# Kernel tuning notes

Measured on AMD Instinct MI355X. Metric: run time of the kernel, lower is better.

Reference implementation:

```python
import jax, jax.numpy as jnp
import numpy as np

B, K, D = 16384, 5, 512
HG = 16  # WeightGate hidden dim
BN_EPS = 1e-5
NORM_EPS = 1e-12  # F.normalize eps


def setup_inputs() -> dict:
    key = jax.random.key(0)
    ks = jax.random.split(key, 10)
    n = jax.random.normal
    s = 0.05
    return {
        "image_embedding": n(ks[0], (B, D), dtype=jnp.float32),
        "text_embeddings": n(ks[1], (B, K, D), dtype=jnp.float32),
        # WeightGate: Linear(1,16) -> ReLU -> Linear(16,1) -> Sigmoid
        "wg_w1": n(ks[2], (1, HG)) * s, "wg_b1": jnp.zeros((HG,)),
        "wg_w2": n(ks[3], (HG, 1)) * s, "wg_b2": jnp.zeros((1,)),
        # MergeGate: Conv2d(1,1,(K,1)) + BN(512) -> Linear(512,512) -> GELU
        "conv_w": n(ks[4], (K,)) * s, "conv_b": jnp.zeros(()),
        "mg_bn_g": jnp.ones((D,)), "mg_bn_b": jnp.zeros((D,)),
        "mg_w": n(ks[5], (D, D)) * s, "mg_b": jnp.zeros((D,)),
        # ProjectionHead (shared for image & text): BN->Linear->GELU->BN->Linear
        "ph_bn1_g": jnp.ones((D,)), "ph_bn1_b": jnp.zeros((D,)),
        "ph_w1": n(ks[6], (D, D)) * s, "ph_b1": jnp.zeros((D,)),
        "ph_bn2_g": jnp.ones((D,)), "ph_bn2_b": jnp.zeros((D,)),
        "ph_w2": n(ks[7], (D, D)) * s, "ph_b2": jnp.zeros((D,)),
    }


def _batchnorm(x, g, b):
    # training-mode BatchNorm1d: batch mean, biased variance
    m = jnp.mean(x, axis=0)
    v = jnp.var(x, axis=0)
    return (x - m) * jax.lax.rsqrt(v + BN_EPS) * g + b


def _l2norm_rows(x):
    return x / jnp.sqrt(jnp.sum(x * x, axis=1, keepdims=True))


def _forward(image_embedding, text_embeddings,
             wg_w1, wg_b1, wg_w2, wg_b2,
             conv_w, conv_b, mg_bn_g, mg_bn_b, mg_w, mg_b,
             ph_bn1_g, ph_bn1_b, ph_w1, ph_b1, ph_bn2_g, ph_bn2_b, ph_w2, ph_b2):
    # cosine similarity: [B, K]
    img_n = image_embedding / jnp.maximum(
        jnp.linalg.norm(image_embedding, axis=-1, keepdims=True), NORM_EPS)
    txt_n = text_embeddings / jnp.maximum(
        jnp.linalg.norm(text_embeddings, axis=-1, keepdims=True), NORM_EPS)
    sim = jnp.einsum("bd,bkd->bk", img_n, txt_n)

    # WeightGate: per-scalar tiny MLP
    h = jax.nn.relu(sim[..., None] * wg_w1[0] + wg_b1)        # [B, K, HG]
    weights = jax.nn.sigmoid(h @ wg_w2 + wg_b2)[..., 0]       # [B, K]

    weighted = text_embeddings * weights[..., None]           # [B, K, D]

    # sort by weight (descending) and gather
    idx = jnp.argsort(-weights, axis=1)                       # [B, K]
    sorted_txt = jnp.take_along_axis(weighted, idx[..., None], axis=1)

    # MergeGate: (K,1) conv collapses K -> scalar weighted sum over K
    x = jnp.einsum("bkd,k->bd", sorted_txt, conv_w) + conv_b  # [B, D]
    # dropout is identity in eval mode
    fused = jax.nn.gelu(_batchnorm(x, mg_bn_g, mg_bn_b) @ mg_w + mg_b)

    def proj(z):
        z = jax.nn.gelu(_batchnorm(z, ph_bn1_g, ph_bn1_b) @ ph_w1 + ph_b1)
        z = _batchnorm(z, ph_bn2_g, ph_bn2_b) @ ph_w2 + ph_b2
        return _l2norm_rows(z)

    return proj(image_embedding), proj(fused)


def reference(image_embedding, text_embeddings,
              wg_w1, wg_b1, wg_w2, wg_b2,
              conv_w, conv_b, mg_bn_g, mg_bn_b, mg_w, mg_b,
              ph_bn1_g, ph_bn1_b, ph_w1, ph_b1, ph_bn2_g, ph_bn2_b, ph_w2, ph_b2):
    return _forward(image_embedding, text_embeddings,
                    wg_w1, wg_b1, wg_w2, wg_b2,
                    conv_w, conv_b, mg_bn_g, mg_bn_b, mg_w, mg_b,
                    ph_bn1_g, ph_bn1_b, ph_w1, ph_b1,
                    ph_bn2_g, ph_bn2_b, ph_w2, ph_b2)
```

## Files before the change

kernel.cpp:

```cpp
#include <hip/hip_runtime.h>
#include <cmath>

#define NROWS 16384
#define DDIM  512

typedef __attribute__((ext_vector_type(8))) short          bf16x8;
typedef __attribute__((ext_vector_type(4))) float          f32x4;
typedef __attribute__((ext_vector_type(8))) unsigned short u16x8;
typedef __attribute__((ext_vector_type(4))) unsigned short u16x4;

__device__ __forceinline__ unsigned short f2bf(float f) {
  unsigned u = __float_as_uint(f);
  u += 0x7fffu + ((u >> 16) & 1u);
  return (unsigned short)(u >> 16);
}

__device__ __forceinline__ float gelu_tanh(float x) {
  float x3 = x * x * x;
  float t = tanhf(0.79788456080286535588f * (x + 0.044715f * x3));
  return 0.5f * x * (1.0f + t);
}

__device__ __forceinline__ void ld8(const float* p, float* v) {
  float4 a = *(const float4*)p;
  float4 b = *(const float4*)(p + 256);
  v[0] = a.x; v[1] = a.y; v[2] = a.z; v[3] = a.w;
  v[4] = b.x; v[5] = b.y; v[6] = b.z; v[7] = b.w;
}

__device__ __forceinline__ void st8(float* p, const float* v) {
  *(float4*)p = make_float4(v[0], v[1], v[2], v[3]);
  *(float4*)(p + 256) = make_float4(v[4], v[5], v[6], v[7]);
}

__device__ __forceinline__ float wave_sum(float v) {
#pragma unroll
  for (int m = 1; m < 64; m <<= 1) v += __shfl_xor(v, m, 64);
  return v;
}

__device__ __forceinline__ void gload_lds16(const void* g, void* l) {
  __builtin_amdgcn_global_load_lds(
      (const __attribute__((address_space(1))) unsigned int*)g,
      (__attribute__((address_space(3))) unsigned int*)l, 16, 0, 0);
}

__global__ __launch_bounds__(256) void prep_kernel(
    const float* __restrict__ img, const float* __restrict__ txt,
    const float* __restrict__ wg_w1, const float* __restrict__ wg_b1,
    const float* __restrict__ wg_w2, const float* __restrict__ wg_b2,
    const float* __restrict__ conv_w, const float* __restrict__ conv_b,
    unsigned short* __restrict__ xbf, unsigned short* __restrict__ imgbf,
    float* __restrict__ accPart) {
  __shared__ float csX[512], cqX[512], csI[512], cqI[512];
  const int tid = threadIdx.x;
  for (int i = tid; i < 512; i += 256) {
    csX[i] = 0.f; cqX[i] = 0.f; csI[i] = 0.f; cqI[i] = 0.f;
  }
  __syncthreads();

  const int lane = tid & 63;
  const int gwave = blockIdx.x * 4 + (tid >> 6);

  const float cb = conv_b[0];
  const float b2f = wg_b2[0];
  float w1f[16], b1f[16], w2f[16];
#pragma unroll
  for (int i = 0; i < 16; i++) {
    w1f[i] = wg_w1[i]; b1f[i] = wg_b1[i]; w2f[i] = wg_w2[i];
  }
  float cw[5];
#pragma unroll
  for (int k = 0; k < 5; k++) cw[k] = conv_w[k];

  float sX[8] = {0, 0, 0, 0, 0, 0, 0, 0}, qX[8] = {0, 0, 0, 0, 0, 0, 0, 0};
  float sI[8] = {0, 0, 0, 0, 0, 0, 0, 0}, qI[8] = {0, 0, 0, 0, 0, 0, 0, 0};

  for (int it = 0; it < 8; it++) {
    const int r = gwave * 8 + it;
    const float* ip = img + (size_t)r * DDIM + lane * 4;
    float iv[8];
    ld8(ip, iv);

    {
      u16x4 lo, hi;
#pragma unroll
      for (int j = 0; j < 4; j++) { lo[j] = f2bf(iv[j]); hi[j] = f2bf(iv[4 + j]); }
      *(u16x4*)(imgbf + (size_t)r * DDIM + lane * 4) = lo;
      *(u16x4*)(imgbf + (size_t)r * DDIM + 256 + lane * 4) = hi;
    }
#pragma unroll
    for (int j = 0; j < 8; j++) { sI[j] += iv[j]; qI[j] += iv[j] * iv[j]; }

    float tv[5][8];
#pragma unroll
    for (int k = 0; k < 5; k++)
      ld8(txt + ((size_t)r * 5 + k) * DDIM + lane * 4, tv[k]);

    double ss = 0.0;
    double s2[5], dp[5];
#pragma unroll
    for (int k = 0; k < 5; k++) { s2[k] = 0.0; dp[k] = 0.0; }
#pragma unroll
    for (int j = 0; j < 8; j++) {
      ss += (double)iv[j] * (double)iv[j];
#pragma unroll
      for (int k = 0; k < 5; k++) {
        s2[k] += (double)tv[k][j] * (double)tv[k][j];
        dp[k] += (double)iv[j] * (double)tv[k][j];
      }
    }

#pragma unroll
    for (int m = 1; m < 64; m <<= 1) {
      ss += __shfl_xor(ss, m, 64);
#pragma unroll
      for (int k = 0; k < 5; k++) {
        s2[k] += __shfl_xor(s2[k], m, 64);
        dp[k] += __shfl_xor(dp[k], m, 64);
      }
    }
    const double dimg = fmax(sqrt(ss), 1e-12);

    double simv[5];
#pragma unroll
    for (int k = 0; k < 5; k++) {
      const double dt = fmax(sqrt(s2[k]), 1e-12);
      simv[k] = dp[k] / (dimg * dt);
    }

    double o[5];
#pragma unroll
    for (int k = 0; k < 5; k++) o[k] = (double)b2f;
#pragma unroll
    for (int i = 0; i < 16; i++) {
      const double w1d = (double)w1f[i];
      const double b1d = (double)b1f[i];
      const double w2d = (double)w2f[i];
#pragma unroll
      for (int k = 0; k < 5; k++) {
        double h = simv[k] * w1d + b1d;
        h = fmax(h, 0.0);
        o[k] += h * w2d;
      }
    }
    float wv[5];
#pragma unroll
    for (int k = 0; k < 5; k++) {
      float o32 = (float)o[k];
      float e32 = (float)exp(-(double)o32);
      float a32 = 1.0f + e32;
      wv[k] = 1.0f / a32;
    }

    float c[5];
#pragma unroll
    for (int k = 0; k < 5; k++) {
      int rk = 0;
#pragma unroll
      for (int j = 0; j < 5; j++)
        rk += (int)((wv[j] > wv[k]) || ((wv[j] == wv[k]) && (j < k)));
      c[k] = cw[rk] * wv[k];
    }

    float xv[8];
#pragma unroll
    for (int j = 0; j < 8; j++) {
      float v = cb;
#pragma unroll
      for (int k = 0; k < 5; k++) v = fmaf(c[k], tv[k][j], v);
      xv[j] = v;
    }
    {
      u16x4 lo, hi;
#pragma unroll
      for (int j = 0; j < 4; j++) { lo[j] = f2bf(xv[j]); hi[j] = f2bf(xv[4 + j]); }
      *(u16x4*)(xbf + (size_t)r * DDIM + lane * 4) = lo;
      *(u16x4*)(xbf + (size_t)r * DDIM + 256 + lane * 4) = hi;
    }

#pragma unroll
    for (int j = 0; j < 8; j++) { sX[j] += xv[j]; qX[j] += xv[j] * xv[j]; }
  }

  const int c0 = lane * 4, c1 = 256 + lane * 4;
#pragma unroll
  for (int j = 0; j < 4; j++) {
    atomicAdd(&csX[c0 + j], sX[j]);     atomicAdd(&cqX[c0 + j], qX[j]);
    atomicAdd(&csX[c1 + j], sX[4 + j]); atomicAdd(&cqX[c1 + j], qX[4 + j]);
    atomicAdd(&csI[c0 + j], sI[j]);     atomicAdd(&cqI[c0 + j], qI[j]);
    atomicAdd(&csI[c1 + j], sI[4 + j]); atomicAdd(&cqI[c1 + j], qI[4 + j]);
  }
  __syncthreads();
  float* base = accPart + (size_t)(blockIdx.x & 31) * 2048;
  for (int i = tid; i < 512; i += 256) {
    atomicAdd(&base[i], csX[i]);
    atomicAdd(&base[512 + i], cqX[i]);
    atomicAdd(&base[1024 + i], csI[i]);
    atomicAdd(&base[1536 + i], cqI[i]);
  }
}

__global__ __launch_bounds__(256) void wconv_kernel(
    const float* __restrict__ W,
    const float* __restrict__ s, const float* __restrict__ q,
    const float* __restrict__ g, const float* __restrict__ b,
    float invM, int ncopies, int stride,
    unsigned short* __restrict__ Wt, float* __restrict__ addv) {
  __shared__ float T[32][33];
  __shared__ float P[32];
  __shared__ float SC[32], SH[32];
  const int t = threadIdx.x;
  const int k0 = blockIdx.x * 32, n0 = blockIdx.y * 32;
  {
    int r = t >> 3, c = (t & 7) * 4;
    float4 v = *(const float4*)&W[(size_t)(k0 + r) * 512 + n0 + c];
    T[r][c] = v.x; T[r][c + 1] = v.y; T[r][c + 2] = v.z; T[r][c + 3] = v.w;
  }
  if (t < 32) {
    P[t] = 0.f;
    const int j = k0 + t;
    float ss = 0.f, qq = 0.f;
    for (int c = 0; c < ncopies; c++) {
      ss += s[(size_t)c * stride + j];
      qq += q[(size_t)c * stride + j];
    }
    float m = ss * invM;
    float v = qq * invM - m * m;
    float r = 1.0f / sqrtf(v + 1e-5f);
    float sc = g[j] * r;
    SC[t] = sc;
    SH[t] = fmaf(-m, sc, b[j]);
  }
  __syncthreads();
  {
    int n = t >> 3, k = (t & 7) * 4;
    u16x4 o;
#pragma unroll
    for (int i = 0; i < 4; i++) o[i] = f2bf(T[k + i][n] * SC[k + i]);
    *(u16x4*)&Wt[(size_t)(n0 + n) * 512 + k0 + k] = o;
  }
  {
    int n = t & 31, rb = (t >> 5) * 4;
    float p = 0.f;
#pragma unroll
    for (int i = 0; i < 4; i++) p += SH[rb + i] * T[rb + i][n];
    atomicAdd(&P[n], p);
  }
  __syncthreads();
  if (t < 32) atomicAdd(&addv[n0 + t], P[t]);
}

__global__ __launch_bounds__(256) void gemm_bf16(
    const unsigned short* __restrict__ A, const unsigned short* __restrict__ Wt,
    const float* __restrict__ bias, const float* __restrict__ addv,
    float* __restrict__ Cf, unsigned short* __restrict__ Cb, int do_gelu,
    float* __restrict__ accS, float* __restrict__ accQ,
    const unsigned short* __restrict__ A2, const unsigned short* __restrict__ W2,
    const float* __restrict__ bias2, const float* __restrict__ addv2,
    float* __restrict__ Cf2, int mblocks) {
  __shared__ __align__(16) short As[128 * 32];
  __shared__ __align__(16) short Bs[128 * 32];
  __shared__ float colS[128], colQ[128];
  const int tid = threadIdx.x;
  const int ln = tid & 63;
  const int lq = ln >> 4, lr = ln & 15;
  const int wv = tid >> 6;
  const int wm = wv >> 1, wn = wv & 1;

  int bx = blockIdx.x;
  if (A2 && bx >= mblocks) {
    bx -= mblocks;
    A = A2; Wt = W2; bias = bias2; addv = addv2; Cf = Cf2; Cb = nullptr;
  }
  const int bm = bx * 128, bn = blockIdx.y * 128;

  f32x4 acc[4][4];
#pragma unroll
  for (int i = 0; i < 4; i++)
#pragma unroll
    for (int j = 0; j < 4; j++) acc[i][j] = (f32x4){0.f, 0.f, 0.f, 0.f};

  const int idx0 = tid, idx1 = 256 + tid;
  const int r0 = idx0 >> 2, k0g = (idx0 & 3) ^ ((r0 >> 1) & 3);
  const int r1 = idx1 >> 2, k1g = (idx1 & 3) ^ ((r1 >> 1) & 3);
  const unsigned short* ga0 = A + (size_t)(bm + r0) * 512 + k0g * 8;
  const unsigned short* ga1 = A + (size_t)(bm + r1) * 512 + k1g * 8;
  const unsigned short* gb0 = Wt + (size_t)(bn + r0) * 512 + k0g * 8;
  const unsigned short* gb1 = Wt + (size_t)(bn + r1) * 512 + k1g * 8;

  const int wb = (tid >> 6) << 10;
  char* lA0 = (char*)As + wb;
  char* lA1 = (char*)As + 4096 + wb;
  char* lB0 = (char*)Bs + wb;
  char* lB1 = (char*)Bs + 4096 + wb;

  gload_lds16(ga0, lA0); gload_lds16(ga1, lA1);
  gload_lds16(gb0, lB0); gload_lds16(gb1, lB1);

  for (int kk = 0; kk < 512; kk += 32) {
    __syncthreads();
    bf16x8 af[4], bfr[4];
#pragma unroll
    for (int i = 0; i < 4; i++) {
      int r = wm * 64 + i * 16 + lr;
      af[i] = *(const bf16x8*)((const char*)As + r * 64 + ((lq ^ ((r >> 1) & 3)) << 4));
    }
#pragma unroll
    for (int j = 0; j < 4; j++) {
      int n = wn * 64 + j * 16 + lr;
      bfr[j] = *(const bf16x8*)((const char*)Bs + n * 64 + ((lq ^ ((n >> 1) & 3)) << 4));
    }
#pragma unroll
    for (int i = 0; i < 4; i++)
#pragma unroll
      for (int j = 0; j < 4; j++)
        acc[i][j] = __builtin_amdgcn_mfma_f32_16x16x32_bf16(af[i], bfr[j], acc[i][j], 0, 0, 0);
    __syncthreads();
    if (kk + 32 < 512) {
      gload_lds16(ga0 + kk + 32, lA0); gload_lds16(ga1 + kk + 32, lA1);
      gload_lds16(gb0 + kk + 32, lB0); gload_lds16(gb1 + kk + 32, lB1);
    }
  }

  const bool do_stats = (accS != nullptr);
  if (do_stats) {
    if (tid < 128) { colS[tid] = 0.f; colQ[tid] = 0.f; }
    __syncthreads();
  }
  float badd[4];
  int cols[4];
#pragma unroll
  for (int j = 0; j < 4; j++) {
    int c = bn + wn * 64 + j * 16 + lr;
    cols[j] = c;
    badd[j] = bias[c] + addv[c];
  }
#pragma unroll
  for (int j = 0; j < 4; j++) {
    float s = 0.f, q = 0.f;
#pragma unroll
    for (int i = 0; i < 4; i++) {
      int rbase = bm + wm * 64 + i * 16 + lq * 4;
#pragma unroll
      for (int rg = 0; rg < 4; rg++) {
        float v = acc[i][j][rg] + badd[j];
        if (do_gelu) v = gelu_tanh(v);
        size_t off = (size_t)(rbase + rg) * 512 + cols[j];
        if (Cb) Cb[off] = f2bf(v);
        else Cf[off] = v;
        s += v; q += v * v;
      }
    }
    if (do_stats) {
      atomicAdd(&colS[wn * 64 + j * 16 + lr], s);
      atomicAdd(&colQ[wn * 64 + j * 16 + lr], q);
    }
  }
  if (do_stats) {
    __syncthreads();
    if (tid < 128) {
      atomicAdd(&accS[bn + tid], colS[tid]);
      atomicAdd(&accQ[bn + tid], colQ[tid]);
    }
  }
}

__global__ __launch_bounds__(256) void l2norm_kernel(float* __restrict__ out) {
  const int wave = blockIdx.x * 4 + (threadIdx.x >> 6);
  const int lane = threadIdx.x & 63;
  float* p = out + (size_t)wave * DDIM + lane * 4;
  float v[8];
  ld8(p, v);
  float ss = 0.f;
#pragma unroll
  for (int j = 0; j < 8; j++) ss += v[j] * v[j];
  ss = wave_sum(ss);
  const float inv = 1.0f / sqrtf(ss);
#pragma unroll
  for (int j = 0; j < 8; j++) v[j] *= inv;
  st8(p, v);
}

extern "C" void kernel_launch(void* const* d_in, const int* in_sizes, int n_in,
                              void* d_out, int out_size, void* d_ws, size_t ws_size,
                              hipStream_t stream) {
  const float* img     = (const float*)d_in[0];
  const float* txt     = (const float*)d_in[1];
  const float* wg_w1   = (const float*)d_in[2];
  const float* wg_b1   = (const float*)d_in[3];
  const float* wg_w2   = (const float*)d_in[4];
  const float* wg_b2   = (const float*)d_in[5];
  const float* conv_w  = (const float*)d_in[6];
  const float* conv_b  = (const float*)d_in[7];
  const float* mg_bn_g = (const float*)d_in[8];
  const float* mg_bn_b = (const float*)d_in[9];
  const float* mg_w    = (const float*)d_in[10];
  const float* mg_b    = (const float*)d_in[11];
  const float* ph_bn1_g= (const float*)d_in[12];
  const float* ph_bn1_b= (const float*)d_in[13];
  const float* ph_w1   = (const float*)d_in[14];
  const float* ph_b1   = (const float*)d_in[15];
  const float* ph_bn2_g= (const float*)d_in[16];
  const float* ph_bn2_b= (const float*)d_in[17];
  const float* ph_w2   = (const float*)d_in[18];
  const float* ph_b2   = (const float*)d_in[19];
  float* out = (float*)d_out;

  const size_t BD = (size_t)NROWS * DDIM;
  const size_t WSZ = 512 * 512;

  unsigned short* xbf   = (unsigned short*)d_ws;
  unsigned short* imgbf = xbf + BD;
  unsigned short* fusbf = imgbf + BD;
  unsigned short* Wt0   = fusbf + BD;
  unsigned short* Wt1   = Wt0 + WSZ;
  unsigned short* Wt2   = Wt1 + WSZ;
  unsigned short* Wt3   = Wt2 + WSZ;
  unsigned short* Wt4   = Wt3 + WSZ;
  float* acc  = (float*)(Wt4 + WSZ);
  float* addv = acc + 10 * 512;
  float* accPart = addv + 5 * 512;

  float* accFs = acc + 4 * 512, *accFq = acc + 5 * 512;
  float* accT1s= acc + 6 * 512, *accT1q= acc + 7 * 512;
  float* accT2s= acc + 8 * 512, *accT2q= acc + 9 * 512;
  float* add0 = addv + 0 * 512, *add1 = addv + 1 * 512, *add2 = addv + 2 * 512;
  float* add3 = addv + 3 * 512, *add4 = addv + 4 * 512;

  hipMemsetAsync(acc, 0, (15 * 512 + 32 * 2048) * sizeof(float), stream);

  prep_kernel<<<512, 256, 0, stream>>>(img, txt, wg_w1, wg_b1, wg_w2, wg_b2,
                                       conv_w, conv_b, xbf, imgbf, accPart);
  const float invM = 1.0f / (float)NROWS;

  dim3 wgrid(16, 16);
  dim3 ggrid(NROWS / 128, DDIM / 128);
  dim3 dgrid(2 * NROWS / 128, DDIM / 128);

  wconv_kernel<<<wgrid, 256, 0, stream>>>(mg_w, accPart + 0, accPart + 512,
                                          mg_bn_g, mg_bn_b, invM, 32, 2048, Wt0, add0);
  wconv_kernel<<<wgrid, 256, 0, stream>>>(ph_w1, accPart + 1024, accPart + 1536,
                                          ph_bn1_g, ph_bn1_b, invM, 32, 2048, Wt1, add1);

  gemm_bf16<<<ggrid, 256, 0, stream>>>(xbf, Wt0, mg_b, add0, nullptr, fusbf, 1,
                                       accFs, accFq,
                                       nullptr, nullptr, nullptr, nullptr, nullptr, 128);
  gemm_bf16<<<ggrid, 256, 0, stream>>>(imgbf, Wt1, ph_b1, add1, nullptr, xbf, 1,
                                       accT1s, accT1q,
                                       nullptr, nullptr, nullptr, nullptr, nullptr, 128);

  wconv_kernel<<<wgrid, 256, 0, stream>>>(ph_w1, accFs, accFq,
                                          ph_bn1_g, ph_bn1_b, invM, 1, 0, Wt2, add2);
  gemm_bf16<<<ggrid, 256, 0, stream>>>(fusbf, Wt2, ph_b1, add2, nullptr, imgbf, 1,
                                       accT2s, accT2q,
                                       nullptr, nullptr, nullptr, nullptr, nullptr, 128);

  wconv_kernel<<<wgrid, 256, 0, stream>>>(ph_w2, accT1s, accT1q,
                                          ph_bn2_g, ph_bn2_b, invM, 1, 0, Wt3, add3);
  wconv_kernel<<<wgrid, 256, 0, stream>>>(ph_w2, accT2s, accT2q,
                                          ph_bn2_g, ph_bn2_b, invM, 1, 0, Wt4, add4);

  gemm_bf16<<<dgrid, 256, 0, stream>>>(xbf, Wt3, ph_b2, add3, out, nullptr, 0,
                                       nullptr, nullptr,
                                       imgbf, Wt4, ph_b2, add4, out + BD, 128);

  l2norm_kernel<<<(2 * NROWS) / 4, 256, 0, stream>>>(out);
}
```

Before: 509.1 us.

## Double-buffer GEMM LDS tiles and merge independent GEMM/wconv launches

The GEMM main loop now uses two LDS buffers, so the next K-slice is loaded while MFMAs run on the current one, with one barrier per iteration instead of two. Independent weight-conversion launches are merged into single launches using the z grid dimension. When the workspace is large enough, independent GEMMs are paired into one launch and the stage order is rearranged, with an extra buffer for the T1 activations. This cuts launch count and idle tail between kernels, at the cost of double the LDS per block and more workspace.

```diff
diff --git a/kernel.cpp b/kernel.cpp
--- a/kernel.cpp
+++ b/kernel.cpp
@@ -202,11 +202,19 @@
 }
 
 __global__ __launch_bounds__(256) void wconv_kernel(
-    const float* __restrict__ W,
-    const float* __restrict__ s, const float* __restrict__ q,
-    const float* __restrict__ g, const float* __restrict__ b,
-    float invM, int ncopies, int stride,
-    unsigned short* __restrict__ Wt, float* __restrict__ addv) {
+    const float* __restrict__ W, const float* __restrict__ s,
+    const float* __restrict__ q, const float* __restrict__ g,
+    const float* __restrict__ b, int ncopies, int stride,
+    unsigned short* __restrict__ Wt, float* __restrict__ addv,
+    const float* __restrict__ W2, const float* __restrict__ s2,
+    const float* __restrict__ q2, const float* __restrict__ g2,
+    const float* __restrict__ b2, int ncopies2, int stride2,
+    unsigned short* __restrict__ Wt2, float* __restrict__ addv2,
+    float invM) {
+  if (blockIdx.z == 1 && W2) {
+    W = W2; s = s2; q = q2; g = g2; b = b2;
+    ncopies = ncopies2; stride = stride2; Wt = Wt2; addv = addv2;
+  }
   __shared__ float T[32][33];
   __shared__ float P[32];
   __shared__ float SC[32], SH[32];
@@ -258,9 +266,10 @@
     float* __restrict__ accS, float* __restrict__ accQ,
     const unsigned short* __restrict__ A2, const unsigned short* __restrict__ W2,
     const float* __restrict__ bias2, const float* __restrict__ addv2,
-    float* __restrict__ Cf2, int mblocks) {
-  __shared__ __align__(16) short As[128 * 32];
-  __shared__ __align__(16) short Bs[128 * 32];
+    float* __restrict__ Cf2, unsigned short* __restrict__ Cb2, int do_gelu2,
+    float* __restrict__ accS2, float* __restrict__ accQ2, int mblocks) {
+  __shared__ __align__(16) short As[2][4096];
+  __shared__ __align__(16) short Bs[2][4096];
   __shared__ float colS[128], colQ[128];
   const int tid = threadIdx.x;
   const int ln = tid & 63;
@@ -271,7 +280,8 @@
   int bx = blockIdx.x;
   if (A2 && bx >= mblocks) {
     bx -= mblocks;
-    A = A2; Wt = W2; bias = bias2; addv = addv2; Cf = Cf2; Cb = nullptr;
+    A = A2; Wt = W2; bias = bias2; addv = addv2; Cf = Cf2; Cb = Cb2;
+    do_gelu = do_gelu2; accS = accS2; accQ = accQ2;
   }
   const int bm = bx * 128, bn = blockIdx.y * 128;
 
@@ -288,28 +298,33 @@
   const unsigned short* ga1 = A + (size_t)(bm + r1) * 512 + k1g * 8;
   const unsigned short* gb0 = Wt + (size_t)(bn + r0) * 512 + k0g * 8;
   const unsigned short* gb1 = Wt + (size_t)(bn + r1) * 512 + k1g * 8;
-
-  const int wb = (tid >> 6) << 10;
-  char* lA0 = (char*)As + wb;
-  char* lA1 = (char*)As + 4096 + wb;
-  char* lB0 = (char*)Bs + wb;
-  char* lB1 = (char*)Bs + 4096 + wb;
-
-  gload_lds16(ga0, lA0); gload_lds16(ga1, lA1);
-  gload_lds16(gb0, lB0); gload_lds16(gb1, lB1);
-
-  for (int kk = 0; kk < 512; kk += 32) {
-    __syncthreads();
+  const int wb = wv << 10;
+
+  gload_lds16(ga0, (char*)As[0] + wb);
+  gload_lds16(ga1, (char*)As[0] + 4096 + wb);
+  gload_lds16(gb0, (char*)Bs[0] + wb);
+  gload_lds16(gb1, (char*)Bs[0] + 4096 + wb);
+  __syncthreads();
+
+  int cur = 0;
+  for (int t = 0; t < 16; ++t) {
+    if (t < 15) {
+      const int ko = (t + 1) * 32;
+      gload_lds16(ga0 + ko, (char*)As[cur ^ 1] + wb);
+      gload_lds16(ga1 + ko, (char*)As[cur ^ 1] + 4096 + wb);
+      gload_lds16(gb0 + ko, (char*)Bs[cur ^ 1] + wb);
+      gload_lds16(gb1 + ko, (char*)Bs[cur ^ 1] + 4096 + wb);
+    }
     bf16x8 af[4], bfr[4];
 #pragma unroll
     for (int i = 0; i < 4; i++) {
       int r = wm * 64 + i * 16 + lr;
-      af[i] = *(const bf16x8*)((const char*)As + r * 64 + ((lq ^ ((r >> 1) & 3)) << 4));
+      af[i] = *(const bf16x8*)((const char*)As[cur] + r * 64 + ((lq ^ ((r >> 1) & 3)) << 4));
     }
 #pragma unroll
     for (int j = 0; j < 4; j++) {
       int n = wn * 64 + j * 16 + lr;
-      bfr[j] = *(const bf16x8*)((const char*)Bs + n * 64 + ((lq ^ ((n >> 1) & 3)) << 4));
+      bfr[j] = *(const bf16x8*)((const char*)Bs[cur] + n * 64 + ((lq ^ ((n >> 1) & 3)) << 4));
     }
 #pragma unroll
     for (int i = 0; i < 4; i++)
@@ -317,10 +332,7 @@
       for (int j = 0; j < 4; j++)
         acc[i][j] = __builtin_amdgcn_mfma_f32_16x16x32_bf16(af[i], bfr[j], acc[i][j], 0, 0, 0);
     __syncthreads();
-    if (kk + 32 < 512) {
-      gload_lds16(ga0 + kk + 32, lA0); gload_lds16(ga1 + kk + 32, lA1);
-      gload_lds16(gb0 + kk + 32, lB0); gload_lds16(gb1 + kk + 32, lB1);
-    }
+    cur ^= 1;
   }
 
   const bool do_stats = (accS != nullptr);
@@ -409,11 +421,17 @@
 
   const size_t BD = (size_t)NROWS * DDIM;
   const size_t WSZ = 512 * 512;
+  const size_t statsF = 15 * 512 + 32 * 2048;
+
+  const size_t need = (4 * BD + 5 * WSZ) * sizeof(unsigned short) +
+                      statsF * sizeof(float);
+  const bool big = ws_size >= need;
 
   unsigned short* xbf   = (unsigned short*)d_ws;
   unsigned short* imgbf = xbf + BD;
   unsigned short* fusbf = imgbf + BD;
-  unsigned short* Wt0   = fusbf + BD;
+  unsigned short* t1b   = big ? fusbf + BD : xbf;
+  unsigned short* Wt0   = big ? fusbf + 2 * BD : fusbf + BD;
   unsigned short* Wt1   = Wt0 + WSZ;
   unsigned short* Wt2   = Wt1 + WSZ;
   unsigned short* Wt3   = Wt2 + WSZ;
@@ -428,42 +446,63 @@
   float* add0 = addv + 0 * 512, *add1 = addv + 1 * 512, *add2 = addv + 2 * 512;
   float* add3 = addv + 3 * 512, *add4 = addv + 4 * 512;
 
-  hipMemsetAsync(acc, 0, (15 * 512 + 32 * 2048) * sizeof(float), stream);
+  hipMemsetAsync(acc, 0, statsF * sizeof(float), stream);
 
   prep_kernel<<<512, 256, 0, stream>>>(img, txt, wg_w1, wg_b1, wg_w2, wg_b2,
                                        conv_w, conv_b, xbf, imgbf, accPart);
   const float invM = 1.0f / (float)NROWS;
 
-  dim3 wgrid(16, 16);
+  dim3 wgrid2(16, 16, 2);
+  dim3 wgrid1(16, 16, 1);
   dim3 ggrid(NROWS / 128, DDIM / 128);
   dim3 dgrid(2 * NROWS / 128, DDIM / 128);
 
-  wconv_kernel<<<wgrid, 256, 0, stream>>>(mg_w, accPart + 0, accPart + 512,
-                                          mg_bn_g, mg_bn_b, invM, 32, 2048, Wt0, add0);
-  wconv_kernel<<<wgrid, 256, 0, stream>>>(ph_w1, accPart + 1024, accPart + 1536,
-                                          ph_bn1_g, ph_bn1_b, invM, 32, 2048, Wt1, add1);
-
-  gemm_bf16<<<ggrid, 256, 0, stream>>>(xbf, Wt0, mg_b, add0, nullptr, fusbf, 1,
-                                       accFs, accFq,
-                                       nullptr, nullptr, nullptr, nullptr, nullptr, 128);
-  gemm_bf16<<<ggrid, 256, 0, stream>>>(imgbf, Wt1, ph_b1, add1, nullptr, xbf, 1,
-                                       accT1s, accT1q,
-                                       nullptr, nullptr, nullptr, nullptr, nullptr, 128);
-
-  wconv_kernel<<<wgrid, 256, 0, stream>>>(ph_w1, accFs, accFq,
-                                          ph_bn1_g, ph_bn1_b, invM, 1, 0, Wt2, add2);
-  gemm_bf16<<<ggrid, 256, 0, stream>>>(fusbf, Wt2, ph_b1, add2, nullptr, imgbf, 1,
-                                       accT2s, accT2q,
-                                       nullptr, nullptr, nullptr, nullptr, nullptr, 128);
-
-  wconv_kernel<<<wgrid, 256, 0, stream>>>(ph_w2, accT1s, accT1q,
-                                          ph_bn2_g, ph_bn2_b, invM, 1, 0, Wt3, add3);
-  wconv_kernel<<<wgrid, 256, 0, stream>>>(ph_w2, accT2s, accT2q,
-                                          ph_bn2_g, ph_bn2_b, invM, 1, 0, Wt4, add4);
-
-  gemm_bf16<<<dgrid, 256, 0, stream>>>(xbf, Wt3, ph_b2, add3, out, nullptr, 0,
-                                       nullptr, nullptr,
-                                       imgbf, Wt4, ph_b2, add4, out + BD, 128);
+  wconv_kernel<<<wgrid2, 256, 0, stream>>>(
+      mg_w, accPart + 0, accPart + 512, mg_bn_g, mg_bn_b, 32, 2048, Wt0, add0,
+      ph_w1, accPart + 1024, accPart + 1536, ph_bn1_g, ph_bn1_b, 32, 2048, Wt1, add1,
+      invM);
+
+  if (big) {
+    gemm_bf16<<<dgrid, 256, 0, stream>>>(
+        xbf, Wt0, mg_b, add0, nullptr, fusbf, 1, accFs, accFq,
+        imgbf, Wt1, ph_b1, add1, nullptr, t1b, 1, accT1s, accT1q, NROWS / 128);
+    wconv_kernel<<<wgrid2, 256, 0, stream>>>(
+        ph_w1, accFs, accFq, ph_bn1_g, ph_bn1_b, 1, 0, Wt2, add2,
+        ph_w2, accT1s, accT1q, ph_bn2_g, ph_bn2_b, 1, 0, Wt3, add3, invM);
+    gemm_bf16<<<dgrid, 256, 0, stream>>>(
+        fusbf, Wt2, ph_b1, add2, nullptr, imgbf, 1, accT2s, accT2q,
+        t1b, Wt3, ph_b2, add3, out, nullptr, 0, nullptr, nullptr, NROWS / 128);
+    wconv_kernel<<<wgrid1, 256, 0, stream>>>(
+        ph_w2, accT2s, accT2q, ph_bn2_g, ph_bn2_b, 1, 0, Wt4, add4,
+        nullptr, nullptr, nullptr, nullptr, nullptr, 0, 0, nullptr, nullptr, invM);
+    gemm_bf16<<<ggrid, 256, 0, stream>>>(
+        imgbf, Wt4, ph_b2, add4, out + BD, nullptr, 0, nullptr, nullptr,
+        nullptr, nullptr, nullptr, nullptr, nullptr, nullptr, 0, nullptr, nullptr,
+        1 << 30);
+  } else {
+    gemm_bf16<<<ggrid, 256, 0, stream>>>(
+        xbf, Wt0, mg_b, add0, nullptr, fusbf, 1, accFs, accFq,
+        nullptr, nullptr, nullptr, nullptr, nullptr, nullptr, 0, nullptr, nullptr,
+        1 << 30);
+    gemm_bf16<<<ggrid, 256, 0, stream>>>(
+        imgbf, Wt1, ph_b1, add1, nullptr, xbf, 1, accT1s, accT1q,
+        nullptr, nullptr, nullptr, nullptr, nullptr, nullptr, 0, nullptr, nullptr,
+        1 << 30);
+    wconv_kernel<<<wgrid2, 256, 0, stream>>>(
+        ph_w1, accFs, accFq, ph_bn1_g, ph_bn1_b, 1, 0, Wt2, add2,
+        ph_w2, accT1s, accT1q, ph_bn2_g, ph_bn2_b, 1, 0, Wt3, add3, invM);
+    gemm_bf16<<<ggrid, 256, 0, stream>>>(
+        fusbf, Wt2, ph_b1, add2, nullptr, imgbf, 1, accT2s, accT2q,
+        nullptr, nullptr, nullptr, nullptr, nullptr, nullptr, 0, nullptr, nullptr,
+        1 << 30);
+    wconv_kernel<<<wgrid1, 256, 0, stream>>>(
+        ph_w2, accT2s, accT2q, ph_bn2_g, ph_bn2_b, 1, 0, Wt4, add4,
+        nullptr, nullptr, nullptr, nullptr, nullptr, 0, 0, nullptr, nullptr, invM);
+    gemm_bf16<<<dgrid, 256, 0, stream>>>(
+        xbf, Wt3, ph_b2, add3, out, nullptr, 0, nullptr, nullptr,
+        imgbf, Wt4, ph_b2, add4, out + BD, nullptr, 0, nullptr, nullptr,
+        NROWS / 128);
+  }
 
   l2norm_kernel<<<(2 * NROWS) / 4, 256, 0, stream>>>(out);
 }
```

After: 516.9 us. No clear change (+1.5%).
